# Performance work log

Measured on AMD Instinct MI355X. Metric: run time of the kernel, lower is better.

The kernel has to match this reference:

```python
import jax, jax.numpy as jnp
import numpy as np

B, N, D = 32, 2048, 1024


def setup_inputs() -> dict:
    key0 = jax.random.key(0)
    ks = jax.random.split(key0, 9)
    scale = 1.0 / np.sqrt(D)
    query = jax.random.normal(ks[0], (B, D), dtype=jnp.float32)
    key = jax.random.normal(ks[1], (B, N, D), dtype=jnp.float32)
    mask = jax.random.randint(ks[2], (B, N), 0, 2, dtype=jnp.int32)
    W1 = jax.random.uniform(ks[3], (D, D), jnp.float32, -scale, scale)
    b1 = jax.random.uniform(ks[4], (D,), jnp.float32, -scale, scale)
    W2 = jax.random.uniform(ks[5], (D, D), jnp.float32, -scale, scale)
    b2 = jax.random.uniform(ks[6], (D,), jnp.float32, -scale, scale)
    v_w = jax.random.uniform(ks[7], (D,), jnp.float32, -scale, scale)
    v_b = jax.random.uniform(ks[8], (), jnp.float32, -scale, scale)
    return {"query": query, "key": key, "mask": mask,
            "W1": W1, "b1": b1, "W2": W2, "b2": b2, "v_w": v_w, "v_b": v_b}


def reference(query, key, mask, W1, b1, W2, b2, v_w, v_b):
    # key_out: [B, N, D] = key @ W1^T + b1 (nn.Linear convention)
    key_out = jnp.einsum('bnd,ed->bne', key, W1) + b1
    # query_out: [B, D] -> broadcast over N
    query_out = jnp.einsum('bd,ed->be', query, W2) + b2
    h = jnp.tanh(key_out + query_out[:, None, :])  # [B, N, D]
    ui = jnp.einsum('bnd,d->bn', h, v_w) + v_b      # v: D -> 1, squeezed
    ui = jnp.where(mask.astype(bool), ui, -jnp.inf)
    return ui
```

## Files before the change

### kernel.cpp

```cpp
#include <hip/hip_runtime.h>
#include <hip/hip_bf16.h>
#include <math.h>

#define B_ 32
#define N_ 2048
#define D_ 1024
#define M_ (B_ * N_)

typedef float  fx4  __attribute__((ext_vector_type(4)));
typedef __bf16 bf16x8 __attribute__((ext_vector_type(8)));
typedef unsigned short us4 __attribute__((ext_vector_type(4)));

#define WS_W1B   134217728ULL
#define WS_T     136314880ULL
#define WS_ACC   136445952ULL

#define MASK_NEG_SENTINEL (-1.0e30f)

__device__ inline unsigned short f2b(float f) {
    __hip_bfloat16 h = __float2bfloat16(f);
    return *reinterpret_cast<unsigned short*>(&h);
}

__global__ void convert_zero_kernel(const float* __restrict__ key,
                                    const float* __restrict__ W1,
                                    us4* __restrict__ keyb4,
                                    us4* __restrict__ w1b4,
                                    fx4* __restrict__ accum4) {
    const long long KEY4 = (long long)M_ * D_ / 4;
    const long long W14  = (long long)D_ * D_ / 4;
    const long long ACC4 = (long long)M_ / 4;
    const long long total = KEY4 + W14 + ACC4;
    long long idx    = (long long)blockIdx.x * blockDim.x + threadIdx.x;
    long long stride = (long long)gridDim.x * blockDim.x;
    const fx4* key4 = (const fx4*)key;
    const fx4* W14p = (const fx4*)W1;
    for (long long i = idx; i < total; i += stride) {
        if (i < KEY4) {
            fx4 v = key4[i];
            us4 o; o.x = f2b(v.x); o.y = f2b(v.y); o.z = f2b(v.z); o.w = f2b(v.w);
            keyb4[i] = o;
        } else if (i < KEY4 + W14) {
            long long j = i - KEY4;
            fx4 v = W14p[j];
            us4 o; o.x = f2b(v.x); o.y = f2b(v.y); o.z = f2b(v.z); o.w = f2b(v.w);
            w1b4[j] = o;
        } else {
            long long j = i - KEY4 - W14;
            fx4 z = {0.f, 0.f, 0.f, 0.f};
            accum4[j] = z;
        }
    }
}

__global__ void tq_kernel(const float* __restrict__ query,
                          const float* __restrict__ W2,
                          const float* __restrict__ b1,
                          const float* __restrict__ b2,
                          float* __restrict__ t) {
    int tid = threadIdx.x;
    int b = tid & 31;
    int e = blockIdx.x * 8 + (tid >> 5);
    const fx4* q = (const fx4*)(query + (size_t)b * D_);
    const fx4* w = (const fx4*)(W2 + (size_t)e * D_);
    float acc = 0.f;
    for (int k = 0; k < D_ / 4; ++k) {
        fx4 qv = q[k];
        fx4 wv = w[k];
        acc += qv.x * wv.x + qv.y * wv.y + qv.z * wv.z + qv.w * wv.w;
    }
    t[(size_t)b * D_ + e] = acc + b2[e] + b1[e];
}

__device__ inline float fast_tanh(float x) {
    float ax = fabsf(x);
    float e  = __expf(-2.0f * ax);
    float r  = (1.0f - e) / (1.0f + e);
    return copysignf(r, x);
}

#define BM 128
#define BN 128
#define BK 32

#define GLD16(g, l)                                                        \
    __builtin_amdgcn_global_load_lds(                                      \
        (const __attribute__((address_space(1))) void*)(g),                \
        (__attribute__((address_space(3))) void*)(l), 16, 0, 0)

__global__ void __launch_bounds__(256)
main_gemm(const unsigned short* __restrict__ keyb,
          const unsigned short* __restrict__ w1b,
          const float* __restrict__ t,
          const float* __restrict__ v_w,
          float* __restrict__ accum) {
    __shared__ unsigned short As[BM * BK];
    __shared__ unsigned short Bs[BN * BK];

    const int tid  = threadIdx.x;
    const int lane = tid & 63;
    const int wave = tid >> 6;
    const int quad = lane >> 4;
    const int l15  = lane & 15;
    const int m0 = blockIdx.x * BM;
    const int e0 = blockIdx.y * BN;
    const int mw = (wave >> 1) * 64;
    const int ew = (wave & 1) * 64;

    const int srow  = tid >> 2;
    const int skoff = (tid & 3) * 8;
    const unsigned short* aSrc0 = keyb + (size_t)(m0 + srow) * D_ + skoff;
    const unsigned short* aSrc1 = aSrc0 + (size_t)64 * D_;
    const unsigned short* bSrc0 = w1b + (size_t)(e0 + srow) * D_ + skoff;
    const unsigned short* bSrc1 = bSrc0 + (size_t)64 * D_;
    char* AsB = (char*)As;
    char* BsB = (char*)Bs;
    char* aDst0 = AsB + wave * 1024;
    char* aDst1 = AsB + 4096 + wave * 1024;
    char* bDst0 = BsB + wave * 1024;
    char* bDst1 = BsB + 4096 + wave * 1024;

    fx4 acc[4][4] = {};

    for (int k0 = 0; k0 < D_; k0 += BK) {
        GLD16(aSrc0 + k0, aDst0);
        GLD16(aSrc1 + k0, aDst1);
        GLD16(bSrc0 + k0, bDst0);
        GLD16(bSrc1 + k0, bDst1);
        __syncthreads();

        bf16x8 a[4], b[4];
#pragma unroll
        for (int i = 0; i < 4; ++i) {
            int ml = mw + i * 16 + l15;
            a[i] = *(const bf16x8*)(&As[ml * BK + quad * 8]);
        }
#pragma unroll
        for (int j = 0; j < 4; ++j) {
            int el = ew + j * 16 + l15;
            b[j] = *(const bf16x8*)(&Bs[el * BK + quad * 8]);
        }
#pragma unroll
        for (int i = 0; i < 4; ++i)
#pragma unroll
            for (int j = 0; j < 4; ++j)
                acc[i][j] = __builtin_amdgcn_mfma_f32_16x16x32_bf16(
                    a[i], b[j], acc[i][j], 0, 0, 0);

        __syncthreads();
    }

    const float* trow = t + (size_t)(m0 >> 11) * D_;
    float vwv[4], tqv[4];
#pragma unroll
    for (int j = 0; j < 4; ++j) {
        int e = e0 + ew + j * 16 + l15;
        vwv[j] = v_w[e];
        tqv[j] = trow[e];
    }
#pragma unroll
    for (int i = 0; i < 4; ++i) {
#pragma unroll
        for (int r = 0; r < 4; ++r) {
            float s = 0.f;
#pragma unroll
            for (int j = 0; j < 4; ++j)
                s += vwv[j] * fast_tanh(acc[i][j][r] + tqv[j]);
            s += __shfl_xor(s, 1);
            s += __shfl_xor(s, 2);
            s += __shfl_xor(s, 4);
            s += __shfl_xor(s, 8);
            if (l15 == 0) {
                int m = m0 + mw + i * 16 + quad * 4 + r;
                atomicAdd(&accum[m], s);
            }
        }
    }
}

__global__ void finalize_kernel(const float* __restrict__ accum,
                                const int* __restrict__ mask,
                                const float* __restrict__ v_b,
                                float* __restrict__ out) {
    int i = blockIdx.x * blockDim.x + threadIdx.x;
    if (i < M_) {
        float vb = v_b[0];
        out[i] = mask[i] ? (accum[i] + vb) : MASK_NEG_SENTINEL;
    }
}

extern "C" void kernel_launch(void* const* d_in, const int* in_sizes, int n_in,
                              void* d_out, int out_size, void* d_ws, size_t ws_size,
                              hipStream_t stream) {
    const float* query = (const float*)d_in[0];
    const float* key   = (const float*)d_in[1];
    const int*   mask  = (const int*)d_in[2];
    const float* W1    = (const float*)d_in[3];
    const float* b1    = (const float*)d_in[4];
    const float* W2    = (const float*)d_in[5];
    const float* b2    = (const float*)d_in[6];
    const float* v_w   = (const float*)d_in[7];
    const float* v_b   = (const float*)d_in[8];

    char* ws = (char*)d_ws;
    unsigned short* keyb = (unsigned short*)ws;
    unsigned short* w1b  = (unsigned short*)(ws + WS_W1B);
    float*          t    = (float*)(ws + WS_T);
    float*          acc  = (float*)(ws + WS_ACC);

    convert_zero_kernel<<<4096, 256, 0, stream>>>(key, W1,
                                                  (us4*)keyb, (us4*)w1b, (fx4*)acc);
    tq_kernel<<<128, 256, 0, stream>>>(query, W2, b1, b2, t);
    dim3 g(512, 8);
    main_gemm<<<g, 256, 0, stream>>>(keyb, w1b, t, v_w, acc);
    finalize_kernel<<<M_ / 256, 256, 0, stream>>>(acc, mask, v_b, (float*)d_out);
}
```

Measured before the change: 644.1 us.

## Fuse key bf16 conversion into GEMM with double-buffered LDS pipeline

The separate pass that converted the whole 256MB fp32 key tensor to bf16 (and wrote 128MB back) is removed. The GEMM now loads fp32 key rows into registers, converts them, and stores them into a double-buffered LDS tile while the MFMAs for the current tile run; W1 still arrives via global_load_lds. The tq kernel is reworked to use 8 lanes per output with a shuffle reduction, and the accumulator is zeroed with a memset. In exchange, each of the 8 column-block tiles re-reads fp32 key, doubling the bytes per reload, and the kernel uses more registers and LDS.

New measurement: 675.7 us. +4.9%, slower.

```diff
diff --git a/kernel.cpp b/kernel.cpp
--- a/kernel.cpp
+++ b/kernel.cpp
@@ -10,10 +10,10 @@
 typedef float  fx4  __attribute__((ext_vector_type(4)));
 typedef __bf16 bf16x8 __attribute__((ext_vector_type(8)));
 typedef unsigned short us4 __attribute__((ext_vector_type(4)));
-
-#define WS_W1B   134217728ULL
-#define WS_T     136314880ULL
-#define WS_ACC   136445952ULL
+typedef unsigned short us8 __attribute__((ext_vector_type(8)));
+
+#define WS_T     2097152ULL
+#define WS_ACC   2228224ULL
 
 #define MASK_NEG_SENTINEL (-1.0e30f)
 
@@ -22,34 +22,15 @@
     return *reinterpret_cast<unsigned short*>(&h);
 }
 
-__global__ void convert_zero_kernel(const float* __restrict__ key,
-                                    const float* __restrict__ W1,
-                                    us4* __restrict__ keyb4,
-                                    us4* __restrict__ w1b4,
-                                    fx4* __restrict__ accum4) {
-    const long long KEY4 = (long long)M_ * D_ / 4;
-    const long long W14  = (long long)D_ * D_ / 4;
-    const long long ACC4 = (long long)M_ / 4;
-    const long long total = KEY4 + W14 + ACC4;
-    long long idx    = (long long)blockIdx.x * blockDim.x + threadIdx.x;
-    long long stride = (long long)gridDim.x * blockDim.x;
-    const fx4* key4 = (const fx4*)key;
-    const fx4* W14p = (const fx4*)W1;
-    for (long long i = idx; i < total; i += stride) {
-        if (i < KEY4) {
-            fx4 v = key4[i];
-            us4 o; o.x = f2b(v.x); o.y = f2b(v.y); o.z = f2b(v.z); o.w = f2b(v.w);
-            keyb4[i] = o;
-        } else if (i < KEY4 + W14) {
-            long long j = i - KEY4;
-            fx4 v = W14p[j];
-            us4 o; o.x = f2b(v.x); o.y = f2b(v.y); o.z = f2b(v.z); o.w = f2b(v.w);
-            w1b4[j] = o;
-        } else {
-            long long j = i - KEY4 - W14;
-            fx4 z = {0.f, 0.f, 0.f, 0.f};
-            accum4[j] = z;
-        }
+__global__ void w1_convert_kernel(const fx4* __restrict__ W1,
+                                  us4* __restrict__ w1b4) {
+    int idx = blockIdx.x * blockDim.x + threadIdx.x;
+#pragma unroll
+    for (int i = 0; i < 4; ++i) {
+        int j = idx + i * 65536;
+        fx4 v = W1[j];
+        us4 o; o.x = f2b(v.x); o.y = f2b(v.y); o.z = f2b(v.z); o.w = f2b(v.w);
+        w1b4[j] = o;
     }
 }
 
@@ -59,17 +40,24 @@
                           const float* __restrict__ b2,
                           float* __restrict__ t) {
     int tid = threadIdx.x;
-    int b = tid & 31;
-    int e = blockIdx.x * 8 + (tid >> 5);
-    const fx4* q = (const fx4*)(query + (size_t)b * D_);
-    const fx4* w = (const fx4*)(W2 + (size_t)e * D_);
+    int p = blockIdx.x * 32 + (tid >> 3);
+    int j = tid & 7;
+    int b = p >> 10;
+    int e = p & 1023;
+    const fx4* q = (const fx4*)query + (size_t)b * 256;
+    const fx4* w = (const fx4*)W2 + (size_t)e * 256;
     float acc = 0.f;
-    for (int k = 0; k < D_ / 4; ++k) {
-        fx4 qv = q[k];
-        fx4 wv = w[k];
+#pragma unroll 4
+    for (int it = 0; it < 32; ++it) {
+        int k4 = it * 8 + j;
+        fx4 qv = q[k4];
+        fx4 wv = w[k4];
         acc += qv.x * wv.x + qv.y * wv.y + qv.z * wv.z + qv.w * wv.w;
     }
-    t[(size_t)b * D_ + e] = acc + b2[e] + b1[e];
+    acc += __shfl_xor(acc, 1);
+    acc += __shfl_xor(acc, 2);
+    acc += __shfl_xor(acc, 4);
+    if (j == 0) t[p] = acc + b1[e] + b2[e];
 }
 
 __device__ inline float fast_tanh(float x) {
@@ -82,6 +70,8 @@
 #define BM 128
 #define BN 128
 #define BK 32
+#define NITER (D_ / BK)
+#define BUFB  8192
 
 #define GLD16(g, l)                                                        \
     __builtin_amdgcn_global_load_lds(                                      \
@@ -89,13 +79,13 @@
         (__attribute__((address_space(3))) void*)(l), 16, 0, 0)
 
 __global__ void __launch_bounds__(256)
-main_gemm(const unsigned short* __restrict__ keyb,
+main_gemm(const float* __restrict__ key,
           const unsigned short* __restrict__ w1b,
           const float* __restrict__ t,
           const float* __restrict__ v_w,
           float* __restrict__ accum) {
-    __shared__ unsigned short As[BM * BK];
-    __shared__ unsigned short Bs[BN * BK];
+    __shared__ unsigned short As[2 * BM * BK];
+    __shared__ unsigned short Bs[2 * BM * BK];
 
     const int tid  = threadIdx.x;
     const int lane = tid & 63;
@@ -109,37 +99,58 @@
 
     const int srow  = tid >> 2;
     const int skoff = (tid & 3) * 8;
-    const unsigned short* aSrc0 = keyb + (size_t)(m0 + srow) * D_ + skoff;
-    const unsigned short* aSrc1 = aSrc0 + (size_t)64 * D_;
+    const float* aSrc0 = key + (size_t)(m0 + srow) * D_ + skoff;
+    const float* aSrc1 = aSrc0 + (size_t)64 * D_;
     const unsigned short* bSrc0 = w1b + (size_t)(e0 + srow) * D_ + skoff;
     const unsigned short* bSrc1 = bSrc0 + (size_t)64 * D_;
+
     char* AsB = (char*)As;
     char* BsB = (char*)Bs;
-    char* aDst0 = AsB + wave * 1024;
-    char* aDst1 = AsB + 4096 + wave * 1024;
-    char* bDst0 = BsB + wave * 1024;
-    char* bDst1 = BsB + 4096 + wave * 1024;
+    const int aOff = tid * 16;
 
     fx4 acc[4][4] = {};
-
-    for (int k0 = 0; k0 < D_; k0 += BK) {
-        GLD16(aSrc0 + k0, aDst0);
-        GLD16(aSrc1 + k0, aDst1);
-        GLD16(bSrc0 + k0, bDst0);
-        GLD16(bSrc1 + k0, bDst1);
+    fx4 rA[4];
+
+    GLD16(bSrc0, BsB + wave * 1024 + lane * 16);
+    GLD16(bSrc1, BsB + 4096 + wave * 1024 + lane * 16);
+    rA[0] = *(const fx4*)(aSrc0);
+    rA[1] = *(const fx4*)(aSrc0 + 4);
+    rA[2] = *(const fx4*)(aSrc1);
+    rA[3] = *(const fx4*)(aSrc1 + 4);
+    {
+        us8 o0, o1;
+        o0[0]=f2b(rA[0].x); o0[1]=f2b(rA[0].y); o0[2]=f2b(rA[0].z); o0[3]=f2b(rA[0].w);
+        o0[4]=f2b(rA[1].x); o0[5]=f2b(rA[1].y); o0[6]=f2b(rA[1].z); o0[7]=f2b(rA[1].w);
+        o1[0]=f2b(rA[2].x); o1[1]=f2b(rA[2].y); o1[2]=f2b(rA[2].z); o1[3]=f2b(rA[2].w);
+        o1[4]=f2b(rA[3].x); o1[5]=f2b(rA[3].y); o1[6]=f2b(rA[3].z); o1[7]=f2b(rA[3].w);
+        *(us8*)(AsB + aOff) = o0;
+        *(us8*)(AsB + 4096 + aOff) = o1;
+    }
+
+    int cur = 0;
+    for (int k = 0; k < NITER; ++k) {
         __syncthreads();
-
+        const int nxt = cur ^ 1;
+        const bool more = (k + 1 < NITER);
+        if (more) {
+            const int ko = (k + 1) * BK;
+            GLD16(bSrc0 + ko, BsB + nxt * BUFB + wave * 1024 + lane * 16);
+            GLD16(bSrc1 + ko, BsB + nxt * BUFB + 4096 + wave * 1024 + lane * 16);
+            rA[0] = *(const fx4*)(aSrc0 + ko);
+            rA[1] = *(const fx4*)(aSrc0 + ko + 4);
+            rA[2] = *(const fx4*)(aSrc1 + ko);
+            rA[3] = *(const fx4*)(aSrc1 + ko + 4);
+        }
+
+        const unsigned short* Ac = As + cur * (BM * BK);
+        const unsigned short* Bc = Bs + cur * (BM * BK);
         bf16x8 a[4], b[4];
 #pragma unroll
-        for (int i = 0; i < 4; ++i) {
-            int ml = mw + i * 16 + l15;
-            a[i] = *(const bf16x8*)(&As[ml * BK + quad * 8]);
-        }
-#pragma unroll
-        for (int j = 0; j < 4; ++j) {
-            int el = ew + j * 16 + l15;
-            b[j] = *(const bf16x8*)(&Bs[el * BK + quad * 8]);
-        }
+        for (int i = 0; i < 4; ++i)
+            a[i] = *(const bf16x8*)(&Ac[(mw + i * 16 + l15) * BK + quad * 8]);
+#pragma unroll
+        for (int j = 0; j < 4; ++j)
+            b[j] = *(const bf16x8*)(&Bc[(ew + j * 16 + l15) * BK + quad * 8]);
 #pragma unroll
         for (int i = 0; i < 4; ++i)
 #pragma unroll
@@ -147,7 +158,16 @@
                 acc[i][j] = __builtin_amdgcn_mfma_f32_16x16x32_bf16(
                     a[i], b[j], acc[i][j], 0, 0, 0);
 
-        __syncthreads();
+        if (more) {
+            us8 o0, o1;
+            o0[0]=f2b(rA[0].x); o0[1]=f2b(rA[0].y); o0[2]=f2b(rA[0].z); o0[3]=f2b(rA[0].w);
+            o0[4]=f2b(rA[1].x); o0[5]=f2b(rA[1].y); o0[6]=f2b(rA[1].z); o0[7]=f2b(rA[1].w);
+            o1[0]=f2b(rA[2].x); o1[1]=f2b(rA[2].y); o1[2]=f2b(rA[2].z); o1[3]=f2b(rA[2].w);
+            o1[4]=f2b(rA[3].x); o1[5]=f2b(rA[3].y); o1[6]=f2b(rA[3].z); o1[7]=f2b(rA[3].w);
+            *(us8*)(AsB + nxt * BUFB + aOff) = o0;
+            *(us8*)(AsB + nxt * BUFB + 4096 + aOff) = o1;
+        }
+        cur = nxt;
     }
 
     const float* trow = t + (size_t)(m0 >> 11) * D_;
@@ -203,15 +223,14 @@
     const float* v_b   = (const float*)d_in[8];
 
     char* ws = (char*)d_ws;
-    unsigned short* keyb = (unsigned short*)ws;
-    unsigned short* w1b  = (unsigned short*)(ws + WS_W1B);
-    float*          t    = (float*)(ws + WS_T);
-    float*          acc  = (float*)(ws + WS_ACC);
-
-    convert_zero_kernel<<<4096, 256, 0, stream>>>(key, W1,
-                                                  (us4*)keyb, (us4*)w1b, (fx4*)acc);
-    tq_kernel<<<128, 256, 0, stream>>>(query, W2, b1, b2, t);
+    unsigned short* w1b = (unsigned short*)ws;
+    float*          t   = (float*)(ws + WS_T);
+    float*          acc = (float*)(ws + WS_ACC);
+
+    w1_convert_kernel<<<256, 256, 0, stream>>>((const fx4*)W1, (us4*)w1b);
+    tq_kernel<<<1024, 256, 0, stream>>>(query, W2, b1, b2, t);
+    hipMemsetAsync(acc, 0, (size_t)M_ * sizeof(float), stream);
     dim3 g(512, 8);
-    main_gemm<<<g, 256, 0, stream>>>(keyb, w1b, t, v_w, acc);
+    main_gemm<<<g, 256, 0, stream>>>(key, w1b, t, v_w, acc);
     finalize_kernel<<<M_ / 256, 256, 0, stream>>>(acc, mask, v_b, (float*)d_out);
 }
```

## Split convert kernel, parallelize query projection, and swap GEMM grid order

Applied to the files above, without the earlier changes.

The fused convert/zero kernel is split into a key converter, a dedicated W1 converter and a hipMemsetAsync for the accumulator, which removes per-element branching and 64-bit indexing. The query-projection kernel now gives each output 8 lanes that split the reduction and combine with shuffles, launching 1024 blocks instead of 128 so more of the GPU is busy. The main GEMM grid is transposed so the 8 column tiles sharing one key row-tile launch next to each other, which should improve L2 reuse of the key tile. The cost is extra kernel launches.

New measurement: 611.3 us. -5.1%, faster.

```diff
diff --git a/kernel.cpp b/kernel.cpp
--- a/kernel.cpp
+++ b/kernel.cpp
@@ -22,34 +22,27 @@
     return *reinterpret_cast<unsigned short*>(&h);
 }
 
-__global__ void convert_zero_kernel(const float* __restrict__ key,
-                                    const float* __restrict__ W1,
-                                    us4* __restrict__ keyb4,
-                                    us4* __restrict__ w1b4,
-                                    fx4* __restrict__ accum4) {
-    const long long KEY4 = (long long)M_ * D_ / 4;
-    const long long W14  = (long long)D_ * D_ / 4;
-    const long long ACC4 = (long long)M_ / 4;
-    const long long total = KEY4 + W14 + ACC4;
-    long long idx    = (long long)blockIdx.x * blockDim.x + threadIdx.x;
-    long long stride = (long long)gridDim.x * blockDim.x;
-    const fx4* key4 = (const fx4*)key;
-    const fx4* W14p = (const fx4*)W1;
-    for (long long i = idx; i < total; i += stride) {
-        if (i < KEY4) {
-            fx4 v = key4[i];
-            us4 o; o.x = f2b(v.x); o.y = f2b(v.y); o.z = f2b(v.z); o.w = f2b(v.w);
-            keyb4[i] = o;
-        } else if (i < KEY4 + W14) {
-            long long j = i - KEY4;
-            fx4 v = W14p[j];
-            us4 o; o.x = f2b(v.x); o.y = f2b(v.y); o.z = f2b(v.z); o.w = f2b(v.w);
-            w1b4[j] = o;
-        } else {
-            long long j = i - KEY4 - W14;
-            fx4 z = {0.f, 0.f, 0.f, 0.f};
-            accum4[j] = z;
-        }
+__global__ void key_convert_kernel(const fx4* __restrict__ key4,
+                                   us4* __restrict__ keyb4) {
+    const int total = 16777216;
+    int idx    = blockIdx.x * blockDim.x + threadIdx.x;
+    int stride = gridDim.x * blockDim.x;
+    for (int i = idx; i < total; i += stride) {
+        fx4 v = key4[i];
+        us4 o; o.x = f2b(v.x); o.y = f2b(v.y); o.z = f2b(v.z); o.w = f2b(v.w);
+        keyb4[i] = o;
+    }
+}
+
+__global__ void w1_convert_kernel(const fx4* __restrict__ W1,
+                                  us4* __restrict__ w1b4) {
+    int idx = blockIdx.x * blockDim.x + threadIdx.x;
+#pragma unroll
+    for (int i = 0; i < 4; ++i) {
+        int j = idx + i * 65536;
+        fx4 v = W1[j];
+        us4 o; o.x = f2b(v.x); o.y = f2b(v.y); o.z = f2b(v.z); o.w = f2b(v.w);
+        w1b4[j] = o;
     }
 }
 
@@ -59,17 +52,24 @@
                           const float* __restrict__ b2,
                           float* __restrict__ t) {
     int tid = threadIdx.x;
-    int b = tid & 31;
-    int e = blockIdx.x * 8 + (tid >> 5);
-    const fx4* q = (const fx4*)(query + (size_t)b * D_);
-    const fx4* w = (const fx4*)(W2 + (size_t)e * D_);
+    int p = blockIdx.x * 32 + (tid >> 3);
+    int j = tid & 7;
+    int b = p >> 10;
+    int e = p & 1023;
+    const fx4* q = (const fx4*)query + (size_t)b * 256;
+    const fx4* w = (const fx4*)W2 + (size_t)e * 256;
     float acc = 0.f;
-    for (int k = 0; k < D_ / 4; ++k) {
-        fx4 qv = q[k];
-        fx4 wv = w[k];
+#pragma unroll 4
+    for (int it = 0; it < 32; ++it) {
+        int k4 = it * 8 + j;
+        fx4 qv = q[k4];
+        fx4 wv = w[k4];
         acc += qv.x * wv.x + qv.y * wv.y + qv.z * wv.z + qv.w * wv.w;
     }
-    t[(size_t)b * D_ + e] = acc + b2[e] + b1[e];
+    acc += __shfl_xor(acc, 1);
+    acc += __shfl_xor(acc, 2);
+    acc += __shfl_xor(acc, 4);
+    if (j == 0) t[p] = acc + b1[e] + b2[e];
 }
 
 __device__ inline float fast_tanh(float x) {
@@ -102,8 +102,8 @@
     const int wave = tid >> 6;
     const int quad = lane >> 4;
     const int l15  = lane & 15;
-    const int m0 = blockIdx.x * BM;
-    const int e0 = blockIdx.y * BN;
+    const int m0 = blockIdx.y * BM;
+    const int e0 = blockIdx.x * BN;
     const int mw = (wave >> 1) * 64;
     const int ew = (wave & 1) * 64;
 
@@ -208,10 +208,11 @@
     float*          t    = (float*)(ws + WS_T);
     float*          acc  = (float*)(ws + WS_ACC);
 
-    convert_zero_kernel<<<4096, 256, 0, stream>>>(key, W1,
-                                                  (us4*)keyb, (us4*)w1b, (fx4*)acc);
-    tq_kernel<<<128, 256, 0, stream>>>(query, W2, b1, b2, t);
-    dim3 g(512, 8);
+    key_convert_kernel<<<4096, 256, 0, stream>>>((const fx4*)key, (us4*)keyb);
+    w1_convert_kernel<<<256, 256, 0, stream>>>((const fx4*)W1, (us4*)w1b);
+    tq_kernel<<<1024, 256, 0, stream>>>(query, W2, b1, b2, t);
+    hipMemsetAsync(acc, 0, (size_t)M_ * sizeof(float), stream);
+    dim3 g(8, 512);
     main_gemm<<<g, 256, 0, stream>>>(keyb, w1b, t, v_w, acc);
     finalize_kernel<<<M_ / 256, 256, 0, stream>>>(acc, mask, v_b, (float*)d_out);
 }
```
